# Kernel tuning notes

Hardware: AMD Instinct MI355X
Metric: run time of the kernel (lower is better)

The kernel has to match this reference:

```python
import jax, jax.numpy as jnp
from jax import lax
import numpy as np

B, C, H, W = 16, 64, 256, 256
K = 3
PAD = (K - 1) // 2


def setup_inputs() -> dict:
    key = jax.random.key(0)
    ks = jax.random.split(key, 5)
    x = jax.random.normal(ks[0], (B, C, H, W), dtype=jnp.float32)
    # conv1: 1x1 conv dim -> dim*k*k, stored as a (C*K*K, C) matrix since input is (b,c,1,1)
    w1 = jax.random.normal(ks[1], (C * K * K, C), dtype=jnp.float32) * 0.1
    b1 = jax.random.normal(ks[2], (C * K * K,), dtype=jnp.float32) * 0.1
    fscale = jax.random.normal(ks[3], (C,), dtype=jnp.float32) * 0.1
    conv_bias = jax.random.normal(ks[4], (C,), dtype=jnp.float32) * 0.1
    return {"x": x, "w1": w1, "b1": b1, "fscale": fscale, "conv_bias": conv_bias}


def reference(x, w1, b1, fscale, conv_bias):
    b, c, h, w = x.shape
    # global average pool -> (b, c)
    avg = x.mean(axis=(2, 3))
    # 1x1 conv on (b,c,1,1) == dense matmul: (b, c*k*k)
    dyn = avg @ w1.T + b1
    # per-sample, per-channel depthwise kernels, sigmoid-gated
    wk = jax.nn.sigmoid(dyn).reshape(b * c, 1, K, K)  # (b*c, 1, k, k)
    # batch folded into channels -> grouped conv with feature_group_count = b*c
    xf = x.reshape(1, b * c, h, w)
    y = lax.conv_general_dilated(
        xf, wk,
        window_strides=(1, 1),
        padding=[(PAD, PAD), (PAD, PAD)],
        feature_group_count=b * c,
        dimension_numbers=("NCHW", "OIHW", "NCHW"),
    )
    y = y.reshape(b, c, h, w) + conv_bias[None, :, None, None]
    # gated residual blend: (x - y) * fscale * x + y
    fs = fscale[None, :, None, None]
    return (x - y) * fs * x + y
```

## Files before the change

### kernel.cpp

```cpp
#include <hip/hip_runtime.h>
#include <math.h>

#define BB 16
#define CC 64
#define HH 256
#define WW 256
#define HWSZ (HH * WW)
#define NP (BB * CC)
#define BAND 64

__global__ __launch_bounds__(256) void mean_kernel(const float* __restrict__ x,
                                                   float* __restrict__ avg) {
    int p = blockIdx.x;
    const float4* xp = (const float4*)(x + (size_t)p * HWSZ);
    float s = 0.f;
    for (int i = threadIdx.x; i < HWSZ / 4; i += 256) {
        float4 v = xp[i];
        s += v.x + v.y + v.z + v.w;
    }
    for (int off = 32; off > 0; off >>= 1) s += __shfl_down(s, off, 64);
    __shared__ float ws[4];
    int lane = threadIdx.x & 63, wid = threadIdx.x >> 6;
    if (lane == 0) ws[wid] = s;
    __syncthreads();
    if (threadIdx.x == 0) {
        avg[p] = (ws[0] + ws[1] + ws[2] + ws[3]) * (1.0f / (float)HWSZ);
    }
}

__global__ __launch_bounds__(256) void wk_kernel(const float* __restrict__ avg,
                                                 const float* __restrict__ w1,
                                                 const float* __restrict__ b1,
                                                 float* __restrict__ wk) {
    int idx = blockIdx.x * 256 + threadIdx.x;
    if (idx >= BB * CC * 9) return;
    int b = idx / (CC * 9);
    int j = idx % (CC * 9);
    const float* a = avg + b * CC;
    const float* wrow = w1 + (size_t)j * CC;
    float s = b1[j];
#pragma unroll
    for (int c2 = 0; c2 < CC; ++c2) s += a[c2] * wrow[c2];
    wk[idx] = 1.0f / (1.0f + expf(-s));
}

__global__ __launch_bounds__(256) void conv_kernel(const float* __restrict__ x,
                                                   const float* __restrict__ wk,
                                                   const float* __restrict__ fscale,
                                                   const float* __restrict__ conv_bias,
                                                   float* __restrict__ out) {
    const int p = blockIdx.y;
    const int band = blockIdx.x;
    const int c = p & (CC - 1);
    const int h0 = band * BAND;
    const float* xp = x + (size_t)p * HWSZ;
    float* op = out + (size_t)p * HWSZ;

    __shared__ float lds[4][WW + 4];
    __shared__ float wsh[9];

    if (threadIdx.x < 9) wsh[threadIdx.x] = wk[p * 9 + threadIdx.x];
    if (threadIdx.x < 4) {
        lds[threadIdx.x][0] = 0.f;
        lds[threadIdx.x][WW + 1] = 0.f;
    }
    const float fs = fscale[c];
    const float cb = conv_bias[c];

    auto load_row = [&](int r) {
        if (threadIdx.x < 64) {
            float4 v;
            if (r >= 0 && r < HH) v = ((const float4*)(xp + r * WW))[threadIdx.x];
            else                  v = make_float4(0.f, 0.f, 0.f, 0.f);
            float* dst = &lds[(r + 4) & 3][1 + threadIdx.x * 4];
            dst[0] = v.x; dst[1] = v.y; dst[2] = v.z; dst[3] = v.w;
        }
    };

    load_row(h0 - 1);
    load_row(h0);
    __syncthreads();

    for (int h = h0; h < h0 + BAND; ++h) {
        load_row(h + 1);
        __syncthreads();
        const int t = threadIdx.x;
        const float* r0 = lds[(h - 1 + 4) & 3];
        const float* r1 = lds[(h + 4) & 3];
        const float* r2 = lds[(h + 1 + 4) & 3];
        float y = cb;
        y += wsh[0] * r0[t] + wsh[1] * r0[t + 1] + wsh[2] * r0[t + 2];
        y += wsh[3] * r1[t] + wsh[4] * r1[t + 1] + wsh[5] * r1[t + 2];
        y += wsh[6] * r2[t] + wsh[7] * r2[t + 1] + wsh[8] * r2[t + 2];
        const float xv = r1[t + 1];
        op[h * WW + t] = (xv - y) * fs * xv + y;
    }
}

extern "C" void kernel_launch(void* const* d_in, const int* in_sizes, int n_in,
                              void* d_out, int out_size, void* d_ws, size_t ws_size,
                              hipStream_t stream) {
    const float* x         = (const float*)d_in[0];
    const float* w1        = (const float*)d_in[1];
    const float* b1        = (const float*)d_in[2];
    const float* fscale    = (const float*)d_in[3];
    const float* conv_bias = (const float*)d_in[4];
    float* out = (float*)d_out;

    float* avg = (float*)d_ws;
    float* wk  = avg + NP;

    mean_kernel<<<NP, 256, 0, stream>>>(x, avg);
    wk_kernel<<<(BB * CC * 9 + 255) / 256, 256, 0, stream>>>(avg, w1, b1, wk);
    dim3 grid(HH / BAND, NP);
    conv_kernel<<<grid, 256, 0, stream>>>(x, wk, fscale, conv_bias, out);
}
```

Measured before the change: 555.6 us.

## Rewrite depthwise conv as per-wave register row streaming with shuffle halos

The conv kernel no longer stages rows in LDS behind a block barrier per row. Each wave now owns a quarter of an image plane and keeps three rows in registers as float4. Horizontal halos come from lane shuffles, and each lane writes four outputs with vectorized stores. The mean kernel is unrolled to issue four independent float4 loads per iteration with separate accumulators. The grid drops to one block per plane, which removes the per-row synchronisation and LDS traffic but cuts the number of blocks and the memory-level parallelism per wave.

```diff
diff --git a/kernel.cpp b/kernel.cpp
--- a/kernel.cpp
+++ b/kernel.cpp
@@ -7,17 +7,23 @@
 #define WW 256
 #define HWSZ (HH * WW)
 #define NP (BB * CC)
-#define BAND 64
 
 __global__ __launch_bounds__(256) void mean_kernel(const float* __restrict__ x,
                                                    float* __restrict__ avg) {
     int p = blockIdx.x;
     const float4* xp = (const float4*)(x + (size_t)p * HWSZ);
-    float s = 0.f;
-    for (int i = threadIdx.x; i < HWSZ / 4; i += 256) {
-        float4 v = xp[i];
-        s += v.x + v.y + v.z + v.w;
+    float s0 = 0.f, s1 = 0.f, s2 = 0.f, s3 = 0.f;
+    for (int i = threadIdx.x; i < HWSZ / 4; i += 1024) {
+        float4 a = xp[i];
+        float4 b = xp[i + 256];
+        float4 c = xp[i + 512];
+        float4 d = xp[i + 768];
+        s0 += a.x + a.y + a.z + a.w;
+        s1 += b.x + b.y + b.z + b.w;
+        s2 += c.x + c.y + c.z + c.w;
+        s3 += d.x + d.y + d.z + d.w;
     }
+    float s = (s0 + s1) + (s2 + s3);
     for (int off = 32; off > 0; off >>= 1) s += __shfl_down(s, off, 64);
     __shared__ float ws[4];
     int lane = threadIdx.x & 63, wid = threadIdx.x >> 6;
@@ -49,51 +55,61 @@
                                                    const float* __restrict__ fscale,
                                                    const float* __restrict__ conv_bias,
                                                    float* __restrict__ out) {
-    const int p = blockIdx.y;
-    const int band = blockIdx.x;
+    const int p = blockIdx.x;
+    const int wave = threadIdx.x >> 6;
+    const int lane = threadIdx.x & 63;
     const int c = p & (CC - 1);
-    const int h0 = band * BAND;
+    const int h0 = wave * (HH / 4);
     const float* xp = x + (size_t)p * HWSZ;
     float* op = out + (size_t)p * HWSZ;
 
-    __shared__ float lds[4][WW + 4];
-    __shared__ float wsh[9];
-
-    if (threadIdx.x < 9) wsh[threadIdx.x] = wk[p * 9 + threadIdx.x];
-    if (threadIdx.x < 4) {
-        lds[threadIdx.x][0] = 0.f;
-        lds[threadIdx.x][WW + 1] = 0.f;
-    }
+    float k0 = wk[p * 9 + 0], k1 = wk[p * 9 + 1], k2 = wk[p * 9 + 2];
+    float k3 = wk[p * 9 + 3], k4 = wk[p * 9 + 4], k5 = wk[p * 9 + 5];
+    float k6 = wk[p * 9 + 6], k7 = wk[p * 9 + 7], k8 = wk[p * 9 + 8];
     const float fs = fscale[c];
     const float cb = conv_bias[c];
 
-    auto load_row = [&](int r) {
-        if (threadIdx.x < 64) {
-            float4 v;
-            if (r >= 0 && r < HH) v = ((const float4*)(xp + r * WW))[threadIdx.x];
-            else                  v = make_float4(0.f, 0.f, 0.f, 0.f);
-            float* dst = &lds[(r + 4) & 3][1 + threadIdx.x * 4];
-            dst[0] = v.x; dst[1] = v.y; dst[2] = v.z; dst[3] = v.w;
-        }
+    auto ldrow = [&](int r) -> float4 {
+        if ((unsigned)r < (unsigned)HH) return ((const float4*)(xp + r * WW))[lane];
+        return make_float4(0.f, 0.f, 0.f, 0.f);
     };
+    auto haloL = [&](float w) { float v = __shfl_up(w, 1, 64); return lane == 0 ? 0.f : v; };
+    auto haloR = [&](float v0) { float v = __shfl_down(v0, 1, 64); return lane == 63 ? 0.f : v; };
 
-    load_row(h0 - 1);
-    load_row(h0);
-    __syncthreads();
+    float4 rp = ldrow(h0 - 1);
+    float4 rc = ldrow(h0);
+    float4 rn = ldrow(h0 + 1);
+    float lp = haloL(rp.w), Rp = haloR(rp.x);
+    float lc = haloL(rc.w), Rc = haloR(rc.x);
 
-    for (int h = h0; h < h0 + BAND; ++h) {
-        load_row(h + 1);
-        __syncthreads();
-        const int t = threadIdx.x;
-        const float* r0 = lds[(h - 1 + 4) & 3];
-        const float* r1 = lds[(h + 4) & 3];
-        const float* r2 = lds[(h + 1 + 4) & 3];
-        float y = cb;
-        y += wsh[0] * r0[t] + wsh[1] * r0[t + 1] + wsh[2] * r0[t + 2];
-        y += wsh[3] * r1[t] + wsh[4] * r1[t + 1] + wsh[5] * r1[t + 2];
-        y += wsh[6] * r2[t] + wsh[7] * r2[t + 1] + wsh[8] * r2[t + 2];
-        const float xv = r1[t + 1];
-        op[h * WW + t] = (xv - y) * fs * xv + y;
+    for (int h = h0; h < h0 + HH / 4; ++h) {
+        float4 rn2 = ldrow(h + 2);
+        float ln = haloL(rn.w), Rn = haloR(rn.x);
+
+        float4 y;
+        y.x = cb + k0 * lp   + k1 * rp.x + k2 * rp.y
+                 + k3 * lc   + k4 * rc.x + k5 * rc.y
+                 + k6 * ln   + k7 * rn.x + k8 * rn.y;
+        y.y = cb + k0 * rp.x + k1 * rp.y + k2 * rp.z
+                 + k3 * rc.x + k4 * rc.y + k5 * rc.z
+                 + k6 * rn.x + k7 * rn.y + k8 * rn.z;
+        y.z = cb + k0 * rp.y + k1 * rp.z + k2 * rp.w
+                 + k3 * rc.y + k4 * rc.z + k5 * rc.w
+                 + k6 * rn.y + k7 * rn.z + k8 * rn.w;
+        y.w = cb + k0 * rp.z + k1 * rp.w + k2 * Rp
+                 + k3 * rc.z + k4 * rc.w + k5 * Rc
+                 + k6 * rn.z + k7 * rn.w + k8 * Rn;
+
+        float4 o;
+        o.x = (rc.x - y.x) * fs * rc.x + y.x;
+        o.y = (rc.y - y.y) * fs * rc.y + y.y;
+        o.z = (rc.z - y.z) * fs * rc.z + y.z;
+        o.w = (rc.w - y.w) * fs * rc.w + y.w;
+        ((float4*)(op + h * WW))[lane] = o;
+
+        rp = rc; rc = rn; rn = rn2;
+        lp = lc; Rp = Rc;
+        lc = ln; Rc = Rn;
     }
 }
 
@@ -112,6 +128,5 @@
 
     mean_kernel<<<NP, 256, 0, stream>>>(x, avg);
     wk_kernel<<<(BB * CC * 9 + 255) / 256, 256, 0, stream>>>(avg, w1, b1, wk);
-    dim3 grid(HH / BAND, NP);
-    conv_kernel<<<grid, 256, 0, stream>>>(x, wk, fscale, conv_bias, out);
+    conv_kernel<<<NP, 256, 0, stream>>>(x, wk, fscale, conv_bias, out);
 }
```

New measurement: 509.2 us. 8.4% less time.
